# Performance work log

Hardware: AMD Instinct MI355X
Metric: run time of the kernel (lower is better)

## Reference

```python
import jax, jax.numpy as jnp
import numpy as np

H = 8          # num_heads
CHUNK = 68     # tokens_per_chunk = blocks_per_chunk(4) * tokens_per_block(17)
EPS = 1e-5


def _layer_norm(t, w, b):
    m = t.mean(-1, keepdims=True)
    v = t.var(-1, keepdims=True)
    return (t - m) / jnp.sqrt(v + EPS) * w + b


def _forward(tokens, embedding, Wq, bq, Wk, bk, Wv, bv, Wg, bg, Wo, bo,
             gn_w, gn_b, ln1_w, ln1_b, ln2_w, ln2_b, w1, b1, w2, b2):
    B, S = tokens.shape
    L, D, _ = Wq.shape
    dh = D // H
    n_chunks = S // CHUNK

    x = embedding[tokens]  # [B,S,D]

    # per-head decay gammas (standard RetNet)
    gamma = 1.0 - 2.0 ** (-5.0 - jnp.arange(H, dtype=jnp.float32))  # [H]

    # rotary relative-position tables (absolute positions, fresh state n=0)
    pos = jnp.arange(S, dtype=jnp.float32)
    inv = 1.0 / (10000.0 ** (jnp.arange(0, dh, 2, dtype=jnp.float32) / dh))
    ang = pos[:, None] * inv[None, :]                      # [S, dh/2]
    cs = jnp.concatenate([jnp.cos(ang)] * 2, -1)[None, :, None, :]  # [1,S,1,dh]
    sn = jnp.concatenate([jnp.sin(ang)] * 2, -1)[None, :, None, :]

    def rot(t):  # t: [B,S,H,dh]
        t1, t2 = jnp.split(t, 2, axis=-1)
        return t * cs + jnp.concatenate([-t2, t1], -1) * sn

    # chunkwise decay structures
    idx = jnp.arange(CHUNK, dtype=jnp.float32)
    expo = idx[:, None] - idx[None, :]
    Dmask = jnp.where(expo >= 0, gamma[:, None, None] ** expo[None], 0.0)  # [H,C,C]
    cross_dec = gamma[None, :] ** (idx[:, None] + 1.0)          # [C,H]
    k_dec = gamma[None, :] ** (CHUNK - 1.0 - idx[:, None])      # [C,H]
    chunk_dec = gamma ** CHUNK                                  # [H]

    for l in range(L):
        h = _layer_norm(x, ln1_w[l], ln1_b[l])
        q = rot((h @ Wq[l] + bq[l]).reshape(B, S, H, dh))
        k = rot((h @ Wk[l] + bk[l]).reshape(B, S, H, dh)) * (dh ** -0.5)
        v = (h @ Wv[l] + bv[l]).reshape(B, S, H, dh)
        # split into chunks, scan carries the per-head KV state [B,H,dh,dh]
        qc = q.reshape(B, n_chunks, CHUNK, H, dh).transpose(1, 0, 2, 3, 4)
        kc = k.reshape(B, n_chunks, CHUNK, H, dh).transpose(1, 0, 2, 3, 4)
        vc = v.reshape(B, n_chunks, CHUNK, H, dh).transpose(1, 0, 2, 3, 4)

        def step(state, qkv):
            qq, kk, vv = qkv  # each [B,C,H,dh]
            inner = jnp.einsum('bihd,bjhd->bhij', qq, kk) * Dmask
            out = jnp.einsum('bhij,bjhd->bihd', inner, vv)
            out = out + jnp.einsum('bihd,bhde->bihe', qq, state) * cross_dec[None, :, :, None]
            state = state * chunk_dec[None, :, None, None] + \
                jnp.einsum('bjhd,bjhe->bhde', kk * k_dec[None, :, :, None], vv)
            return state, out

        state0 = jnp.zeros((B, H, dh, dh), dtype=x.dtype)
        _, ret = jax.lax.scan(step, state0, (qc, kc, vc))
        ret = ret.transpose(1, 0, 2, 3, 4).reshape(B, S, H, dh)
        # per-head group norm
        m = ret.mean(-1, keepdims=True)
        vr = ret.var(-1, keepdims=True)
        ret = (ret - m) / jnp.sqrt(vr + EPS)
        ret = (ret * gn_w[l].reshape(H, dh) + gn_b[l].reshape(H, dh)).reshape(B, S, D)
        g = jax.nn.silu(h @ Wg[l] + bg[l])
        x = x + (g * ret) @ Wo[l] + bo[l]
        h2 = _layer_norm(x, ln2_w[l], ln2_b[l])
        x = x + jax.nn.silu(h2 @ w1[l] + b1[l]) @ w2[l] + b2[l]
    return x


def setup_inputs() -> dict:
    key = jax.random.key(0)
    B, S, D, L, FF, V = 16, 408, 512, 10, 2048, 519
    ks = jax.random.split(key, 16)
    r = lambda i, shape, s=0.02: jax.random.normal(ks[i], shape, dtype=jnp.float32) * s
    return {
        'tokens': jax.random.randint(ks[0], (B, S), 0, V, dtype=jnp.int32),
        'embedding': r(1, (V, D)),
        'Wq': r(2, (L, D, D)), 'bq': jnp.zeros((L, D), jnp.float32),
        'Wk': r(3, (L, D, D)), 'bk': jnp.zeros((L, D), jnp.float32),
        'Wv': r(4, (L, D, D)), 'bv': jnp.zeros((L, D), jnp.float32),
        'Wg': r(5, (L, D, D)), 'bg': jnp.zeros((L, D), jnp.float32),
        'Wo': r(6, (L, D, D)), 'bo': jnp.zeros((L, D), jnp.float32),
        'gn_w': jnp.ones((L, D), jnp.float32), 'gn_b': jnp.zeros((L, D), jnp.float32),
        'ln1_w': jnp.ones((L, D), jnp.float32), 'ln1_b': jnp.zeros((L, D), jnp.float32),
        'ln2_w': jnp.ones((L, D), jnp.float32), 'ln2_b': jnp.zeros((L, D), jnp.float32),
        'w1': r(7, (L, D, FF)), 'b1': jnp.zeros((L, FF), jnp.float32),
        'w2': r(8, (L, FF, D)), 'b2': jnp.zeros((L, D), jnp.float32),
    }


def reference(tokens, embedding, Wq, bq, Wk, bk, Wv, bv, Wg, bg, Wo, bo,
              gn_w, gn_b, ln1_w, ln1_b, ln2_w, ln2_b, w1, b1, w2, b2):
    return _forward(tokens, embedding, Wq, bq, Wk, bk, Wv, bv, Wg, bg, Wo, bo,
                    gn_w, gn_b, ln1_w, ln1_b, ln2_w, ln2_b, w1, b1, w2, b2)
```

## Files before the change

kernel.cpp:

```cpp
#include <hip/hip_runtime.h>
#include <hip/hip_bf16.h>

#define H 8
#define DH 64
#define DMODEL 512
#define SEQ 408
#define BATCH 16
#define NLAYER 10
#define FFDIM 2048
#define CHUNK 68
#define NCHUNK 6
#define M (BATCH*SEQ)
#define EPS 1e-5f

typedef __hip_bfloat16 bf16;
typedef unsigned short ushort_t;
typedef short bf8v __attribute__((ext_vector_type(8)));
typedef float f4v  __attribute__((ext_vector_type(4)));

__device__ __forceinline__ float us2f(unsigned short u){ return __uint_as_float(((unsigned)u) << 16); }
__device__ __forceinline__ unsigned short f2bfs(float f){
  __bf16 h = (__bf16)f;
  return *(unsigned short*)&h;
}
__device__ __forceinline__ void split2(float f, unsigned short& hi, unsigned short& lo){
  hi = f2bfs(f);
  lo = f2bfs(f - us2f(hi));
}

__global__ void embed_kernel(const int* __restrict__ tokens, const float* __restrict__ emb,
                             float* __restrict__ x){
  int idx = blockIdx.x*256 + threadIdx.x;
  if (idx >= M*DMODEL) return;
  int r = idx >> 9; int d = idx & 511;
  x[idx] = emb[(size_t)tokens[r]*DMODEL + d];
}

__global__ __launch_bounds__(256) void ln_kernel(const float* __restrict__ x,
    const float* __restrict__ w, const float* __restrict__ b,
    ushort_t* __restrict__ hhi, ushort_t* __restrict__ hlo){
  __shared__ float red[8];
  int r = blockIdx.x, tid = threadIdx.x;
  size_t base = (size_t)r*DMODEL;
  float v0 = x[base + tid], v1 = x[base + tid + 256];
  float s = v0 + v1, s2 = v0*v0 + v1*v1;
  int lane = tid & 63, wv = tid >> 6;
  #pragma unroll
  for (int o = 32; o; o >>= 1){ s += __shfl_xor(s, o); s2 += __shfl_xor(s2, o); }
  if (lane == 0){ red[wv] = s; red[wv+4] = s2; }
  __syncthreads();
  float tot  = red[0]+red[1]+red[2]+red[3];
  float tot2 = red[4]+red[5]+red[6]+red[7];
  float mean = tot * (1.0f/512.0f);
  float var  = tot2 * (1.0f/512.0f) - mean*mean;
  float rinv = rsqrtf(var + EPS);
  float o0 = (v0-mean)*rinv*w[tid]     + b[tid];
  float o1 = (v1-mean)*rinv*w[tid+256] + b[tid+256];
  unsigned short hi, lo;
  split2(o0, hi, lo); hhi[base+tid] = hi; hlo[base+tid] = lo;
  split2(o1, hi, lo); hhi[base+tid+256] = hi; hlo[base+tid+256] = lo;
}

#define BN 128
#define BK 32
#define LDK 40

template<int TBM>
__global__ __launch_bounds__(256) void gemm_mfma_kernel(
    const ushort_t* __restrict__ Ahi, const ushort_t* __restrict__ Alo,
    const float* __restrict__ W, const float* __restrict__ bias,
    const float* Cin, float* Cout, ushort_t* Co_hi, ushort_t* Co_lo,
    int N, int K, int epi)
{
  constexpr int TM = TBM/32;
  __shared__ __align__(16) short AsH[TBM*LDK];
  __shared__ __align__(16) short AsL[TBM*LDK];
  __shared__ __align__(16) short BsH[BN*LDK];
  __shared__ __align__(16) short BsL[BN*LDK];
  int tid = threadIdx.x;
  int lane = tid & 63, wave = tid >> 6;
  int wm = (wave >> 1) * (TBM/2), wn = (wave & 1) * 64;
  int l15 = lane & 15, quad = lane >> 4;
  int bm = blockIdx.y * TBM, bn = blockIdx.x * BN;

  f4v acc[TM][4];
  #pragma unroll
  for (int i = 0; i < TM; i++)
    #pragma unroll
    for (int j = 0; j < 4; j++) acc[i][j] = (f4v){0.f,0.f,0.f,0.f};

  int arow, akseg;
  if (TBM == 128){ arow = tid >> 1; akseg = (tid & 1) * 16; }
  else           { arow = tid >> 2; akseg = (tid & 3) * 8;  }
  int bnn = tid & 127, bkseg = (tid >> 7) * 16;

  for (int k0 = 0; k0 < K; k0 += BK){
    if (TBM == 128){
      const uint4* ap = (const uint4*)(Ahi + (size_t)(bm + arow)*K + k0 + akseg);
      uint4 a0 = ap[0], a1 = ap[1];
      *(uint4*)&AsH[arow*LDK + akseg]     = a0;
      *(uint4*)&AsH[arow*LDK + akseg + 8] = a1;
      const uint4* lp = (const uint4*)(Alo + (size_t)(bm + arow)*K + k0 + akseg);
      uint4 l0 = lp[0], l1 = lp[1];
      *(uint4*)&AsL[arow*LDK + akseg]     = l0;
      *(uint4*)&AsL[arow*LDK + akseg + 8] = l1;
    } else {
      uint4 a0 = *(const uint4*)(Ahi + (size_t)(bm + arow)*K + k0 + akseg);
      *(uint4*)&AsH[arow*LDK + akseg] = a0;
      uint4 l0 = *(const uint4*)(Alo + (size_t)(bm + arow)*K + k0 + akseg);
      *(uint4*)&AsL[arow*LDK + akseg] = l0;
    }
    size_t wbase = (size_t)(k0 + bkseg)*N + bn + bnn;
    unsigned short whi[16], wlo[16];
    #pragma unroll
    for (int i = 0; i < 16; i++) split2(W[wbase + (size_t)i*N], whi[i], wlo[i]);
    unsigned* bh = (unsigned*)&BsH[bnn*LDK + bkseg];
    unsigned* bl = (unsigned*)&BsL[bnn*LDK + bkseg];
    #pragma unroll
    for (int i = 0; i < 8; i++){
      bh[i] = (unsigned)whi[2*i] | ((unsigned)whi[2*i+1] << 16);
      bl[i] = (unsigned)wlo[2*i] | ((unsigned)wlo[2*i+1] << 16);
    }
    __syncthreads();
    bf8v afh[TM], afl[TM], bfh[4], bfl[4];
    #pragma unroll
    for (int t = 0; t < TM; t++){
      afh[t] = *(const bf8v*)&AsH[(wm + t*16 + l15)*LDK + quad*8];
      afl[t] = *(const bf8v*)&AsL[(wm + t*16 + l15)*LDK + quad*8];
    }
    #pragma unroll
    for (int t = 0; t < 4; t++){
      bfh[t] = *(const bf8v*)&BsH[(wn + t*16 + l15)*LDK + quad*8];
      bfl[t] = *(const bf8v*)&BsL[(wn + t*16 + l15)*LDK + quad*8];
    }
    #pragma unroll
    for (int i = 0; i < TM; i++)
      #pragma unroll
      for (int j = 0; j < 4; j++){
        acc[i][j] = __builtin_amdgcn_mfma_f32_16x16x32_bf16(afh[i], bfl[j], acc[i][j], 0, 0, 0);
        acc[i][j] = __builtin_amdgcn_mfma_f32_16x16x32_bf16(afl[i], bfh[j], acc[i][j], 0, 0, 0);
        acc[i][j] = __builtin_amdgcn_mfma_f32_16x16x32_bf16(afh[i], bfh[j], acc[i][j], 0, 0, 0);
      }
    __syncthreads();
  }
  #pragma unroll
  for (int i = 0; i < TM; i++){
    int m0 = bm + wm + i*16 + quad*4;
    #pragma unroll
    for (int j = 0; j < 4; j++){
      int n = bn + wn + j*16 + l15;
      float bsv = bias[n];
      #pragma unroll
      for (int r = 0; r < 4; r++){
        int m = m0 + r;
        float c = acc[i][j][r] + bsv;
        if (epi == 1) c = c / (1.0f + expf(-c));
        if (epi == 2) c += Cin[(size_t)m*N + n];
        if (Co_hi){
          unsigned short hi, lo; split2(c, hi, lo);
          Co_hi[(size_t)m*N + n] = hi;
          Co_lo[(size_t)m*N + n] = lo;
        } else {
          Cout[(size_t)m*N + n] = c;
        }
      }
    }
  }
}

__global__ __launch_bounds__(256) void gemm_qkvg_kernel(
    const ushort_t* __restrict__ Ahi, const ushort_t* __restrict__ Alo,
    const float* __restrict__ Wq, const float* __restrict__ Wk,
    const float* __restrict__ Wv, const float* __restrict__ Wg,
    const float* __restrict__ bq, const float* __restrict__ bk,
    const float* __restrict__ bv, const float* __restrict__ bg,
    float* __restrict__ qo, float* __restrict__ ko,
    float* __restrict__ vo, float* __restrict__ go)
{
  const int N = DMODEL, K = DMODEL;
  __shared__ __align__(16) short AsH[128*LDK];
  __shared__ __align__(16) short AsL[128*LDK];
  __shared__ __align__(16) short BsH[BN*LDK];
  __shared__ __align__(16) short BsL[BN*LDK];
  int tid = threadIdx.x;
  int lane = tid & 63, wave = tid >> 6;
  int wm = (wave >> 1) * 64, wn = (wave & 1) * 64;
  int l15 = lane & 15, quad = lane >> 4;
  int which = blockIdx.x >> 2;
  int bn = (blockIdx.x & 3) * BN;
  int bm = blockIdx.y * 128;
  const float* W    = (which==0) ? Wq : (which==1) ? Wk : (which==2) ? Wv : Wg;
  const float* bias = (which==0) ? bq : (which==1) ? bk : (which==2) ? bv : bg;
  float* out        = (which==0) ? qo : (which==1) ? ko : (which==2) ? vo : go;

  f4v acc[4][4];
  #pragma unroll
  for (int i = 0; i < 4; i++)
    #pragma unroll
    for (int j = 0; j < 4; j++) acc[i][j] = (f4v){0.f,0.f,0.f,0.f};

  int arow = tid >> 1, akseg = (tid & 1) * 16;
  int bnn = tid & 127, bkseg = (tid >> 7) * 16;

  for (int k0 = 0; k0 < K; k0 += BK){
    {
      const uint4* ap = (const uint4*)(Ahi + (size_t)(bm + arow)*K + k0 + akseg);
      uint4 a0 = ap[0], a1 = ap[1];
      *(uint4*)&AsH[arow*LDK + akseg]     = a0;
      *(uint4*)&AsH[arow*LDK + akseg + 8] = a1;
      const uint4* lp = (const uint4*)(Alo + (size_t)(bm + arow)*K + k0 + akseg);
      uint4 l0 = lp[0], l1 = lp[1];
      *(uint4*)&AsL[arow*LDK + akseg]     = l0;
      *(uint4*)&AsL[arow*LDK + akseg + 8] = l1;
    }
    size_t wbase = (size_t)(k0 + bkseg)*N + bn + bnn;
    unsigned short whi[16], wlo[16];
    #pragma unroll
    for (int i = 0; i < 16; i++) split2(W[wbase + (size_t)i*N], whi[i], wlo[i]);
    unsigned* bh = (unsigned*)&BsH[bnn*LDK + bkseg];
    unsigned* bl = (unsigned*)&BsL[bnn*LDK + bkseg];
    #pragma unroll
    for (int i = 0; i < 8; i++){
      bh[i] = (unsigned)whi[2*i] | ((unsigned)whi[2*i+1] << 16);
      bl[i] = (unsigned)wlo[2*i] | ((unsigned)wlo[2*i+1] << 16);
    }
    __syncthreads();
    bf8v afh[4], afl[4], bfh[4], bfl[4];
    #pragma unroll
    for (int t = 0; t < 4; t++){
      afh[t] = *(const bf8v*)&AsH[(wm + t*16 + l15)*LDK + quad*8];
      afl[t] = *(const bf8v*)&AsL[(wm + t*16 + l15)*LDK + quad*8];
      bfh[t] = *(const bf8v*)&BsH[(wn + t*16 + l15)*LDK + quad*8];
      bfl[t] = *(const bf8v*)&BsL[(wn + t*16 + l15)*LDK + quad*8];
    }
    #pragma unroll
    for (int i = 0; i < 4; i++)
      #pragma unroll
      for (int j = 0; j < 4; j++){
        acc[i][j] = __builtin_amdgcn_mfma_f32_16x16x32_bf16(afh[i], bfl[j], acc[i][j], 0, 0, 0);
        acc[i][j] = __builtin_amdgcn_mfma_f32_16x16x32_bf16(afl[i], bfh[j], acc[i][j], 0, 0, 0);
        acc[i][j] = __builtin_amdgcn_mfma_f32_16x16x32_bf16(afh[i], bfh[j], acc[i][j], 0, 0, 0);
      }
    __syncthreads();
  }
  #pragma unroll
  for (int i = 0; i < 4; i++){
    int m0 = bm + wm + i*16 + quad*4;
    #pragma unroll
    for (int j = 0; j < 4; j++){
      int n = bn + wn + j*16 + l15;
      float bsv = bias[n];
      #pragma unroll
      for (int r = 0; r < 4; r++){
        int m = m0 + r;
        float c = acc[i][j][r] + bsv;
        if (which == 3) c = c / (1.0f + expf(-c));
        out[(size_t)m*N + n] = c;
      }
    }
  }
}

__global__ void rope_kernel(float* __restrict__ q, float* __restrict__ k){
  int idx = blockIdx.x*256 + threadIdx.x;
  if (idx >= M*256) return;
  int r = idx >> 8, p = idx & 255;
  int hh = p >> 5, i = p & 31;
  int s = r % SEQ;
  float inv = powf(10000.0f, -(float)(2*i) * (1.0f/64.0f));
  float ang = (float)s * inv;
  float sn, c; sincosf(ang, &sn, &c);
  size_t base = (size_t)r*DMODEL + hh*64 + i;
  float q1 = q[base], q2 = q[base+32];
  q[base]    = q1*c - q2*sn;
  q[base+32] = q2*c + q1*sn;
  float k1 = k[base], k2 = k[base+32];
  const float sc = 0.125f;
  k[base]    = (k1*c - k2*sn)*sc;
  k[base+32] = (k2*c + k1*sn)*sc;
}

__global__ __launch_bounds__(256) void ret_chunkkv_kernel(
    const float* __restrict__ k, const float* __restrict__ v, float* __restrict__ Ast)
{
  __shared__ __align__(16) float kT[DH][CHUNK];
  __shared__ __align__(16) float vs[CHUNK][DH];
  __shared__ float gpw[CHUNK];
  int tid = threadIdx.x;
  int c = blockIdx.x % NCHUNK;
  int bh = blockIdx.x / NCHUNK;
  int hh = bh & 7, b = bh >> 3;
  float gamma = 1.0f - exp2f(-5.0f - (float)hh);
  if (tid < CHUNK) gpw[tid] = powf(gamma, (float)(CHUNK-1-tid));
  size_t rowbase = ((size_t)(b*SEQ + c*CHUNK))*DMODEL + hh*DH;
  for (int e = tid; e < CHUNK*DH; e += 256){
    int i = e >> 6, d = e & 63;
    size_t g = rowbase + (size_t)i*DMODEL + d;
    kT[d][i] = k[g];
    vs[i][d] = v[g];
  }
  __syncthreads();
  float* A = Ast + (size_t)blockIdx.x * (DH*DH);
  for (int e = tid; e < DH*16; e += 256){
    int d = e >> 4, q4 = (e & 15) * 4;
    float4 a4 = {0,0,0,0};
    for (int j = 0; j < CHUNK; j++){
      float kj = kT[d][j] * gpw[j];
      float4 v4 = *(const float4*)&vs[j][q4];
      a4.x += kj*v4.x; a4.y += kj*v4.y; a4.z += kj*v4.z; a4.w += kj*v4.w;
    }
    *(float4*)&A[d*DH + q4] = a4;
  }
}

__global__ __launch_bounds__(256) void ret_scan_kernel(float* __restrict__ Ast)
{
  int bh = blockIdx.x, hh = bh & 7;
  float gamma = 1.0f - exp2f(-5.0f - (float)hh);
  float chdec = powf(gamma, (float)CHUNK);
  int tid = threadIdx.x;
  float4 run[4];
  #pragma unroll
  for (int t = 0; t < 4; t++) run[t] = (float4){0,0,0,0};
  size_t base = (size_t)bh * NCHUNK * (DH*DH) + (size_t)tid*16;
  for (int c = 0; c < NCHUNK; c++){
    float4* slot = (float4*)(Ast + base + (size_t)c*(DH*DH));
    float4 a[4];
    #pragma unroll
    for (int t = 0; t < 4; t++) a[t] = slot[t];
    #pragma unroll
    for (int t = 0; t < 4; t++) slot[t] = run[t];
    #pragma unroll
    for (int t = 0; t < 4; t++){
      run[t].x = run[t].x*chdec + a[t].x;
      run[t].y = run[t].y*chdec + a[t].y;
      run[t].z = run[t].z*chdec + a[t].z;
      run[t].w = run[t].w*chdec + a[t].w;
    }
  }
}

__global__ __launch_bounds__(256) void ret_out_kernel(
    const float* __restrict__ q, const float* __restrict__ k, const float* __restrict__ v,
    const float* __restrict__ Ast, float* __restrict__ ret)
{
  __shared__ __align__(16) float qs[CHUNK][DH];
  __shared__ __align__(16) float kT[DH][CHUNK];
  __shared__ __align__(16) float vs[CHUNK][DH];
  __shared__ __align__(16) float sts[DH*DH];
  __shared__ float inner[34][CHUNK];
  __shared__ float gpw[CHUNK];
  int tid = threadIdx.x;
  int c = blockIdx.x % NCHUNK;
  int bh = blockIdx.x / NCHUNK;
  int hh = bh & 7, b = bh >> 3;
  float gamma = 1.0f - exp2f(-5.0f - (float)hh);
  if (tid < CHUNK) gpw[tid] = powf(gamma, (float)tid);
  size_t rowbase = ((size_t)(b*SEQ + c*CHUNK))*DMODEL + hh*DH;
  for (int e = tid; e < CHUNK*DH; e += 256){
    int i = e >> 6, d = e & 63;
    size_t g = rowbase + (size_t)i*DMODEL + d;
    qs[i][d] = q[g];
    kT[d][i] = k[g];
    vs[i][d] = v[g];
  }
  const float* st = Ast + (size_t)blockIdx.x * (DH*DH);
  for (int e = tid*4; e < DH*DH; e += 1024)
    *(float4*)&sts[e] = *(const float4*)&st[e];
  __syncthreads();
  for (int p = 0; p < 2; p++){
    int i0 = p*34;
    for (int e = tid; e < 34*CHUNK; e += 256){
      int ii = e / CHUNK, j = e - ii*CHUNK;
      int i = i0 + ii;
      float val = 0.0f;
      if (j <= i){
        float dot = 0.0f;
        #pragma unroll 16
        for (int d = 0; d < DH; d++) dot += qs[i][d] * kT[d][j];
        val = dot * gpw[i-j];
      }
      inner[ii][j] = val;
    }
    __syncthreads();
    for (int e = tid; e < 34*16; e += 256){
      int ii = e >> 4, q4 = (e & 15) * 4;
      int i = i0 + ii;
      float4 o4 = {0,0,0,0};
      for (int j = 0; j <= i; j++){
        float w = inner[ii][j];
        float4 v4 = *(const float4*)&vs[j][q4];
        o4.x += w*v4.x; o4.y += w*v4.y; o4.z += w*v4.z; o4.w += w*v4.w;
      }
      float4 c4 = {0,0,0,0};
      #pragma unroll 8
      for (int e2 = 0; e2 < DH; e2++){
        float qv = qs[i][e2];
        float4 s4 = *(const float4*)&sts[e2*DH + q4];
        c4.x += qv*s4.x; c4.y += qv*s4.y; c4.z += qv*s4.z; c4.w += qv*s4.w;
      }
      float cd = gpw[i] * gamma;
      size_t ob = rowbase + (size_t)i*DMODEL + q4;
      float4 o; o.x = o4.x + cd*c4.x; o.y = o4.y + cd*c4.y;
      o.z = o4.z + cd*c4.z; o.w = o4.w + cd*c4.w;
      *(float4*)&ret[ob] = o;
    }
    __syncthreads();
  }
}

__global__ __launch_bounds__(512) void gnorm_gate_kernel(const float* __restrict__ ret,
    const float* __restrict__ g, const float* __restrict__ gnw, const float* __restrict__ gnb,
    ushort_t* __restrict__ ohi, ushort_t* __restrict__ olo)
{
  int r = blockIdx.x, tid = threadIdx.x;
  size_t idx = (size_t)r*DMODEL + tid;
  float val = ret[idx];
  float s = val, s2 = val*val;
  #pragma unroll
  for (int o = 32; o; o >>= 1){ s += __shfl_xor(s, o); s2 += __shfl_xor(s2, o); }
  float mean = s * (1.0f/64.0f);
  float var  = s2 * (1.0f/64.0f) - mean*mean;
  float y = (val - mean) * rsqrtf(var + EPS);
  y = y * gnw[tid] + gnb[tid];
  y = y * g[idx];
  unsigned short hi, lo; split2(y, hi, lo);
  ohi[idx] = hi; olo[idx] = lo;
}

__global__ void outwrite_kernel(const float* __restrict__ x, float* __restrict__ out){
  int idx = blockIdx.x*256 + threadIdx.x;
  if (idx < M*DMODEL) out[idx] = x[idx];
}

extern "C" void kernel_launch(void* const* d_in, const int* in_sizes, int n_in,
                              void* d_out, int out_size, void* d_ws, size_t ws_size,
                              hipStream_t stream)
{
  (void)in_sizes; (void)n_in; (void)out_size; (void)ws_size;
  const int*   tokens = (const int*)d_in[0];
  const float* emb  = (const float*)d_in[1];
  const float* Wq = (const float*)d_in[2];  const float* bq = (const float*)d_in[3];
  const float* Wk = (const float*)d_in[4];  const float* bk = (const float*)d_in[5];
  const float* Wv = (const float*)d_in[6];  const float* bv = (const float*)d_in[7];
  const float* Wg = (const float*)d_in[8];  const float* bg = (const float*)d_in[9];
  const float* Wo = (const float*)d_in[10]; const float* bo = (const float*)d_in[11];
  const float* gnw = (const float*)d_in[12]; const float* gnb = (const float*)d_in[13];
  const float* ln1w = (const float*)d_in[14]; const float* ln1b = (const float*)d_in[15];
  const float* ln2w = (const float*)d_in[16]; const float* ln2b = (const float*)d_in[17];
  const float* w1 = (const float*)d_in[18]; const float* b1 = (const float*)d_in[19];
  const float* w2 = (const float*)d_in[20]; const float* b2 = (const float*)d_in[21];

  const size_t MD = (size_t)M*DMODEL;
  float* xf = (float*)d_ws;
  float* qf = xf + MD;
  float* kf = qf + MD;
  float* vf = kf + MD;
  float* gf = vf + MD;
  float* rf = gf + MD;
  ushort_t* h_hi = (ushort_t*)(rf + MD);
  ushort_t* h_lo = h_hi + MD;
  float* Ast = (float*)h_hi;
  ushort_t* rg_hi = h_hi;
  ushort_t* rg_lo = h_lo;
  ushort_t* ff_hi = (ushort_t*)qf;
  ushort_t* ff_lo = (ushort_t*)vf;

  embed_kernel<<<(M*DMODEL)/256, 256, 0, stream>>>(tokens, emb, xf);

  dim3 gqkvg(16, M/128);
  dim3 g512b(DMODEL/BN, M/64);
  dim3 gff(FFDIM/BN, M/128);
  for (int l = 0; l < NLAYER; l++){
    const size_t wO = (size_t)l*DMODEL*DMODEL;
    const size_t bO = (size_t)l*DMODEL;
    const size_t w1O = (size_t)l*DMODEL*FFDIM;
    const size_t b1O = (size_t)l*FFDIM;
    ln_kernel<<<M, 256, 0, stream>>>(xf, ln1w + bO, ln1b + bO, h_hi, h_lo);
    gemm_qkvg_kernel<<<gqkvg, 256, 0, stream>>>(h_hi, h_lo,
        Wq + wO, Wk + wO, Wv + wO, Wg + wO,
        bq + bO, bk + bO, bv + bO, bg + bO,
        qf, kf, vf, gf);
    rope_kernel<<<M, 256, 0, stream>>>(qf, kf);
    ret_chunkkv_kernel<<<BATCH*H*NCHUNK, 256, 0, stream>>>(kf, vf, Ast);
    ret_scan_kernel<<<BATCH*H, 256, 0, stream>>>(Ast);
    ret_out_kernel<<<BATCH*H*NCHUNK, 256, 0, stream>>>(qf, kf, vf, Ast, rf);
    gnorm_gate_kernel<<<M, 512, 0, stream>>>(rf, gf, gnw + bO, gnb + bO, rg_hi, rg_lo);
    gemm_mfma_kernel<64><<<g512b, 256, 0, stream>>>(rg_hi, rg_lo, Wo + wO, bo + bO, xf, xf, nullptr, nullptr, DMODEL, DMODEL, 2);
    ln_kernel<<<M, 256, 0, stream>>>(xf, ln2w + bO, ln2b + bO, h_hi, h_lo);
    gemm_mfma_kernel<128><<<gff, 256, 0, stream>>>(h_hi, h_lo, w1 + w1O, b1 + b1O, nullptr, nullptr, ff_hi, ff_lo, FFDIM, DMODEL, 1);
    gemm_mfma_kernel<64><<<g512b, 256, 0, stream>>>(ff_hi, ff_lo, w2 + w1O, b2 + bO, xf, xf, nullptr, nullptr, DMODEL, FFDIM, 2);
  }
  outwrite_kernel<<<(M*DMODEL)/256, 256, 0, stream>>>(xf, (float*)d_out);
}
```

Measured before the change: 4.202 ms.

## Pre-split weights into transposed bf16 hi/lo buffers and prefetch GEMM tiles

Adds per-layer kernels that convert each fp32 weight matrix once into transposed bf16 hi/lo arrays in a workspace. Every GEMM block previously repeated this conversion with strided, uncoalesced loads. The GEMMs now load pre-split weights with vectorized 16-byte reads and register-prefetch the next K tile while computing the current one. The cost is extra split kernel launches and workspace traffic each layer, and the workspace aliases the rf buffer, so its lifetime must not overlap the retention output.

After: 4.126 ms. No clear change (-1.8%).

```diff
diff --git a/kernel.cpp b/kernel.cpp
--- a/kernel.cpp
+++ b/kernel.cpp
@@ -17,6 +17,15 @@
 typedef unsigned short ushort_t;
 typedef short bf8v __attribute__((ext_vector_type(8)));
 typedef float f4v  __attribute__((ext_vector_type(4)));
+
+static constexpr size_t QKVG_STRIDE = 2u*512*512;
+static constexpr size_t QKVG_HL     = 512*512;
+static constexpr size_t WO_HI = 0;
+static constexpr size_t WO_LO = WO_HI + 512*512;
+static constexpr size_t W1_HI = WO_LO + 512*512;
+static constexpr size_t W1_LO = W1_HI + 2048*512;
+static constexpr size_t W2_HI = W1_LO + 2048*512;
+static constexpr size_t W2_LO = W2_HI + 512*2048;
 
 __device__ __forceinline__ float us2f(unsigned short u){ return __uint_as_float(((unsigned)u) << 16); }
 __device__ __forceinline__ unsigned short f2bfs(float f){
@@ -61,14 +70,66 @@
   split2(o1, hi, lo); hhi[base+tid+256] = hi; hlo[base+tid+256] = lo;
 }
 
+__device__ __forceinline__ void wsplit_tile(const float* __restrict__ W,
+    ushort_t* __restrict__ hi, ushort_t* __restrict__ lo,
+    int N, int K, int n0, int k0)
+{
+  __shared__ float tb[32][33];
+  int tx = threadIdx.x & 31, ty = threadIdx.x >> 5;
+  #pragma unroll
+  for (int r = 0; r < 32; r += 8)
+    tb[ty+r][tx] = W[(size_t)(k0+ty+r)*N + n0 + tx];
+  __syncthreads();
+  #pragma unroll
+  for (int r = 0; r < 32; r += 8){
+    float v = tb[tx][ty+r];
+    unsigned short h, l; split2(v, h, l);
+    size_t o = (size_t)(n0+ty+r)*K + k0 + tx;
+    hi[o] = h; lo[o] = l;
+  }
+}
+
+__global__ __launch_bounds__(256) void wsplit_qkvg_kernel(
+    const float* __restrict__ Wq, const float* __restrict__ Wk,
+    const float* __restrict__ Wv, const float* __restrict__ Wg,
+    ushort_t* __restrict__ wsp)
+{
+  int z = blockIdx.z;
+  const float* W = (z==0)?Wq:(z==1)?Wk:(z==2)?Wv:Wg;
+  ushort_t* hi = wsp + (size_t)z*QKVG_STRIDE;
+  wsplit_tile(W, hi, hi + QKVG_HL, 512, 512, blockIdx.x*32, blockIdx.y*32);
+}
+
+__global__ __launch_bounds__(256) void wsplit_ffo_kernel(
+    const float* __restrict__ Wo, const float* __restrict__ w1,
+    const float* __restrict__ w2, ushort_t* __restrict__ wsp)
+{
+  int b = blockIdx.x;
+  const float* W; ushort_t* hi; int N, K, n0, k0;
+  if (b < 256){
+    W = Wo; hi = wsp + WO_HI; N = 512; K = 512;
+    n0 = (b & 15)*32; k0 = (b >> 4)*32;
+  } else if (b < 1280){
+    int bb = b - 256;
+    W = w1; hi = wsp + W1_HI; N = 2048; K = 512;
+    n0 = (bb & 63)*32; k0 = (bb >> 6)*32;
+  } else {
+    int bb = b - 1280;
+    W = w2; hi = wsp + W2_HI; N = 512; K = 2048;
+    n0 = (bb & 15)*32; k0 = (bb >> 4)*32;
+  }
+  wsplit_tile(W, hi, hi + (size_t)N*K, N, K, n0, k0);
+}
+
 #define BN 128
 #define BK 32
 #define LDK 40
 
 template<int TBM>
-__global__ __launch_bounds__(256) void gemm_mfma_kernel(
+__global__ __launch_bounds__(256) void gemm_ps_kernel(
     const ushort_t* __restrict__ Ahi, const ushort_t* __restrict__ Alo,
-    const float* __restrict__ W, const float* __restrict__ bias,
+    const ushort_t* __restrict__ Bhi, const ushort_t* __restrict__ Blo,
+    const float* __restrict__ bias,
     const float* Cin, float* Cout, ushort_t* Co_hi, ushort_t* Co_lo,
     int N, int K, int epi)
 {
@@ -94,44 +155,45 @@
   else           { arow = tid >> 2; akseg = (tid & 3) * 8;  }
   int bnn = tid & 127, bkseg = (tid >> 7) * 16;
 
-  for (int k0 = 0; k0 < K; k0 += BK){
+  const ushort_t* aH = Ahi + (size_t)(bm + arow)*K + akseg;
+  const ushort_t* aL = Alo + (size_t)(bm + arow)*K + akseg;
+  const ushort_t* bH = Bhi + (size_t)(bn + bnn)*K + bkseg;
+  const ushort_t* bL = Blo + (size_t)(bn + bnn)*K + bkseg;
+
+  uint4 rAh0, rAh1, rAl0, rAl1, rBh0, rBh1, rBl0, rBl1;
+#define GLOAD_PS(k0) do{ \
+    rAh0 = *(const uint4*)(aH + (k0)); \
+    rAl0 = *(const uint4*)(aL + (k0)); \
+    if (TBM == 128){ rAh1 = *(const uint4*)(aH + (k0) + 8); \
+                     rAl1 = *(const uint4*)(aL + (k0) + 8); } \
+    rBh0 = *(const uint4*)(bH + (k0));     rBh1 = *(const uint4*)(bH + (k0) + 8); \
+    rBl0 = *(const uint4*)(bL + (k0));     rBl1 = *(const uint4*)(bL + (k0) + 8); \
+  }while(0)
+
+  GLOAD_PS(0);
+  const int nt = K / BK;
+  for (int t = 0; t < nt; t++){
+    __syncthreads();
+    *(uint4*)&AsH[arow*LDK + akseg] = rAh0;
+    *(uint4*)&AsL[arow*LDK + akseg] = rAl0;
     if (TBM == 128){
-      const uint4* ap = (const uint4*)(Ahi + (size_t)(bm + arow)*K + k0 + akseg);
-      uint4 a0 = ap[0], a1 = ap[1];
-      *(uint4*)&AsH[arow*LDK + akseg]     = a0;
-      *(uint4*)&AsH[arow*LDK + akseg + 8] = a1;
-      const uint4* lp = (const uint4*)(Alo + (size_t)(bm + arow)*K + k0 + akseg);
-      uint4 l0 = lp[0], l1 = lp[1];
-      *(uint4*)&AsL[arow*LDK + akseg]     = l0;
-      *(uint4*)&AsL[arow*LDK + akseg + 8] = l1;
-    } else {
-      uint4 a0 = *(const uint4*)(Ahi + (size_t)(bm + arow)*K + k0 + akseg);
-      *(uint4*)&AsH[arow*LDK + akseg] = a0;
-      uint4 l0 = *(const uint4*)(Alo + (size_t)(bm + arow)*K + k0 + akseg);
-      *(uint4*)&AsL[arow*LDK + akseg] = l0;
-    }
-    size_t wbase = (size_t)(k0 + bkseg)*N + bn + bnn;
-    unsigned short whi[16], wlo[16];
-    #pragma unroll
-    for (int i = 0; i < 16; i++) split2(W[wbase + (size_t)i*N], whi[i], wlo[i]);
-    unsigned* bh = (unsigned*)&BsH[bnn*LDK + bkseg];
-    unsigned* bl = (unsigned*)&BsL[bnn*LDK + bkseg];
-    #pragma unroll
-    for (int i = 0; i < 8; i++){
-      bh[i] = (unsigned)whi[2*i] | ((unsigned)whi[2*i+1] << 16);
-      bl[i] = (unsigned)wlo[2*i] | ((unsigned)wlo[2*i+1] << 16);
-    }
+      *(uint4*)&AsH[arow*LDK + akseg + 8] = rAh1;
+      *(uint4*)&AsL[arow*LDK + akseg + 8] = rAl1;
+    }
+    *(uint4*)&BsH[bnn*LDK + bkseg] = rBh0; *(uint4*)&BsH[bnn*LDK + bkseg + 8] = rBh1;
+    *(uint4*)&BsL[bnn*LDK + bkseg] = rBl0; *(uint4*)&BsL[bnn*LDK + bkseg + 8] = rBl1;
     __syncthreads();
+    if (t + 1 < nt) GLOAD_PS((t+1)*BK);
     bf8v afh[TM], afl[TM], bfh[4], bfl[4];
     #pragma unroll
-    for (int t = 0; t < TM; t++){
-      afh[t] = *(const bf8v*)&AsH[(wm + t*16 + l15)*LDK + quad*8];
-      afl[t] = *(const bf8v*)&AsL[(wm + t*16 + l15)*LDK + quad*8];
-    }
-    #pragma unroll
-    for (int t = 0; t < 4; t++){
-      bfh[t] = *(const bf8v*)&BsH[(wn + t*16 + l15)*LDK + quad*8];
-      bfl[t] = *(const bf8v*)&BsL[(wn + t*16 + l15)*LDK + quad*8];
+    for (int i = 0; i < TM; i++){
+      afh[i] = *(const bf8v*)&AsH[(wm + i*16 + l15)*LDK + quad*8];
+      afl[i] = *(const bf8v*)&AsL[(wm + i*16 + l15)*LDK + quad*8];
+    }
+    #pragma unroll
+    for (int j = 0; j < 4; j++){
+      bfh[j] = *(const bf8v*)&BsH[(wn + j*16 + l15)*LDK + quad*8];
+      bfl[j] = *(const bf8v*)&BsL[(wn + j*16 + l15)*LDK + quad*8];
     }
     #pragma unroll
     for (int i = 0; i < TM; i++)
@@ -141,8 +203,8 @@
         acc[i][j] = __builtin_amdgcn_mfma_f32_16x16x32_bf16(afl[i], bfh[j], acc[i][j], 0, 0, 0);
         acc[i][j] = __builtin_amdgcn_mfma_f32_16x16x32_bf16(afh[i], bfh[j], acc[i][j], 0, 0, 0);
       }
-    __syncthreads();
-  }
+  }
+#undef GLOAD_PS
   #pragma unroll
   for (int i = 0; i < TM; i++){
     int m0 = bm + wm + i*16 + quad*4;
@@ -170,8 +232,7 @@
 
 __global__ __launch_bounds__(256) void gemm_qkvg_kernel(
     const ushort_t* __restrict__ Ahi, const ushort_t* __restrict__ Alo,
-    const float* __restrict__ Wq, const float* __restrict__ Wk,
-    const float* __restrict__ Wv, const float* __restrict__ Wg,
+    const ushort_t* __restrict__ wsp,
     const float* __restrict__ bq, const float* __restrict__ bk,
     const float* __restrict__ bv, const float* __restrict__ bg,
     float* __restrict__ qo, float* __restrict__ ko,
@@ -189,7 +250,8 @@
   int which = blockIdx.x >> 2;
   int bn = (blockIdx.x & 3) * BN;
   int bm = blockIdx.y * 128;
-  const float* W    = (which==0) ? Wq : (which==1) ? Wk : (which==2) ? Wv : Wg;
+  const ushort_t* Bhi = wsp + (size_t)which * QKVG_STRIDE;
+  const ushort_t* Blo = Bhi + QKVG_HL;
   const float* bias = (which==0) ? bq : (which==1) ? bk : (which==2) ? bv : bg;
   float* out        = (which==0) ? qo : (which==1) ? ko : (which==2) ? vo : go;
 
@@ -202,36 +264,38 @@
   int arow = tid >> 1, akseg = (tid & 1) * 16;
   int bnn = tid & 127, bkseg = (tid >> 7) * 16;
 
-  for (int k0 = 0; k0 < K; k0 += BK){
-    {
-      const uint4* ap = (const uint4*)(Ahi + (size_t)(bm + arow)*K + k0 + akseg);
-      uint4 a0 = ap[0], a1 = ap[1];
-      *(uint4*)&AsH[arow*LDK + akseg]     = a0;
-      *(uint4*)&AsH[arow*LDK + akseg + 8] = a1;
-      const uint4* lp = (const uint4*)(Alo + (size_t)(bm + arow)*K + k0 + akseg);
-      uint4 l0 = lp[0], l1 = lp[1];
-      *(uint4*)&AsL[arow*LDK + akseg]     = l0;
-      *(uint4*)&AsL[arow*LDK + akseg + 8] = l1;
-    }
-    size_t wbase = (size_t)(k0 + bkseg)*N + bn + bnn;
-    unsigned short whi[16], wlo[16];
-    #pragma unroll
-    for (int i = 0; i < 16; i++) split2(W[wbase + (size_t)i*N], whi[i], wlo[i]);
-    unsigned* bh = (unsigned*)&BsH[bnn*LDK + bkseg];
-    unsigned* bl = (unsigned*)&BsL[bnn*LDK + bkseg];
-    #pragma unroll
-    for (int i = 0; i < 8; i++){
-      bh[i] = (unsigned)whi[2*i] | ((unsigned)whi[2*i+1] << 16);
-      bl[i] = (unsigned)wlo[2*i] | ((unsigned)wlo[2*i+1] << 16);
-    }
+  const ushort_t* aH = Ahi + (size_t)(bm + arow)*K + akseg;
+  const ushort_t* aL = Alo + (size_t)(bm + arow)*K + akseg;
+  const ushort_t* bH = Bhi + (size_t)(bn + bnn)*K + bkseg;
+  const ushort_t* bL = Blo + (size_t)(bn + bnn)*K + bkseg;
+
+  uint4 rAh0, rAh1, rAl0, rAl1, rBh0, rBh1, rBl0, rBl1;
+#define GLOADQ(k0) do{ \
+    rAh0 = *(const uint4*)(aH + (k0)); rAh1 = *(const uint4*)(aH + (k0) + 8); \
+    rAl0 = *(const uint4*)(aL + (k0)); rAl1 = *(const uint4*)(aL + (k0) + 8); \
+    rBh0 = *(const uint4*)(bH + (k0)); rBh1 = *(const uint4*)(bH + (k0) + 8); \
+    rBl0 = *(const uint4*)(bL + (k0)); rBl1 = *(const uint4*)(bL + (k0) + 8); \
+  }while(0)
+
+  GLOADQ(0);
+  const int nt = K / BK;
+  for (int t = 0; t < nt; t++){
     __syncthreads();
+    *(uint4*)&AsH[arow*LDK + akseg]     = rAh0;
+    *(uint4*)&AsH[arow*LDK + akseg + 8] = rAh1;
+    *(uint4*)&AsL[arow*LDK + akseg]     = rAl0;
+    *(uint4*)&AsL[arow*LDK + akseg + 8] = rAl1;
+    *(uint4*)&BsH[bnn*LDK + bkseg] = rBh0; *(uint4*)&BsH[bnn*LDK + bkseg + 8] = rBh1;
+    *(uint4*)&BsL[bnn*LDK + bkseg] = rBl0; *(uint4*)&BsL[bnn*LDK + bkseg + 8] = rBl1;
+    __syncthreads();
+    if (t + 1 < nt) GLOADQ((t+1)*BK);
     bf8v afh[4], afl[4], bfh[4], bfl[4];
     #pragma unroll
-    for (int t = 0; t < 4; t++){
-      afh[t] = *(const bf8v*)&AsH[(wm + t*16 + l15)*LDK + quad*8];
-      afl[t] = *(const bf8v*)&AsL[(wm + t*16 + l15)*LDK + quad*8];
-      bfh[t] = *(const bf8v*)&BsH[(wn + t*16 + l15)*LDK + quad*8];
-      bfl[t] = *(const bf8v*)&BsL[(wn + t*16 + l15)*LDK + quad*8];
+    for (int i = 0; i < 4; i++){
+      afh[i] = *(const bf8v*)&AsH[(wm + i*16 + l15)*LDK + quad*8];
+      afl[i] = *(const bf8v*)&AsL[(wm + i*16 + l15)*LDK + quad*8];
+      bfh[i] = *(const bf8v*)&BsH[(wn + i*16 + l15)*LDK + quad*8];
+      bfl[i] = *(const bf8v*)&BsL[(wn + i*16 + l15)*LDK + quad*8];
     }
     #pragma unroll
     for (int i = 0; i < 4; i++)
@@ -241,8 +305,8 @@
         acc[i][j] = __builtin_amdgcn_mfma_f32_16x16x32_bf16(afl[i], bfh[j], acc[i][j], 0, 0, 0);
         acc[i][j] = __builtin_amdgcn_mfma_f32_16x16x32_bf16(afh[i], bfh[j], acc[i][j], 0, 0, 0);
       }
-    __syncthreads();
-  }
+  }
+#undef GLOADQ
   #pragma unroll
   for (int i = 0; i < 4; i++){
     int m0 = bm + wm + i*16 + quad*4;
@@ -465,20 +529,22 @@
   ushort_t* rg_lo = h_lo;
   ushort_t* ff_hi = (ushort_t*)qf;
   ushort_t* ff_lo = (ushort_t*)vf;
+  ushort_t* wsp = (ushort_t*)rf;
 
   embed_kernel<<<(M*DMODEL)/256, 256, 0, stream>>>(tokens, emb, xf);
 
   dim3 gqkvg(16, M/128);
   dim3 g512b(DMODEL/BN, M/64);
   dim3 gff(FFDIM/BN, M/128);
+  dim3 gsplit4(16, 16, 4);
   for (int l = 0; l < NLAYER; l++){
     const size_t wO = (size_t)l*DMODEL*DMODEL;
     const size_t bO = (size_t)l*DMODEL;
     const size_t w1O = (size_t)l*DMODEL*FFDIM;
     const size_t b1O = (size_t)l*FFDIM;
+    wsplit_qkvg_kernel<<<gsplit4, 256, 0, stream>>>(Wq + wO, Wk + wO, Wv + wO, Wg + wO, wsp);
     ln_kernel<<<M, 256, 0, stream>>>(xf, ln1w + bO, ln1b + bO, h_hi, h_lo);
-    gemm_qkvg_kernel<<<gqkvg, 256, 0, stream>>>(h_hi, h_lo,
-        Wq + wO, Wk + wO, Wv + wO, Wg + wO,
+    gemm_qkvg_kernel<<<gqkvg, 256, 0, stream>>>(h_hi, h_lo, wsp,
         bq + bO, bk + bO, bv + bO, bg + bO,
         qf, kf, vf, gf);
     rope_kernel<<<M, 256, 0, stream>>>(qf, kf);
@@ -486,10 +552,14 @@
     ret_scan_kernel<<<BATCH*H, 256, 0, stream>>>(Ast);
     ret_out_kernel<<<BATCH*H*NCHUNK, 256, 0, stream>>>(qf, kf, vf, Ast, rf);
     gnorm_gate_kernel<<<M, 512, 0, stream>>>(rf, gf, gnw + bO, gnb + bO, rg_hi, rg_lo);
-    gemm_mfma_kernel<64><<<g512b, 256, 0, stream>>>(rg_hi, rg_lo, Wo + wO, bo + bO, xf, xf, nullptr, nullptr, DMODEL, DMODEL, 2);
+    wsplit_ffo_kernel<<<2304, 256, 0, stream>>>(Wo + wO, w1 + w1O, w2 + w1O, wsp);
+    gemm_ps_kernel<64><<<g512b, 256, 0, stream>>>(rg_hi, rg_lo,
+        wsp + WO_HI, wsp + WO_LO, bo + bO, xf, xf, nullptr, nullptr, DMODEL, DMODEL, 2);
     ln_kernel<<<M, 256, 0, stream>>>(xf, ln2w + bO, ln2b + bO, h_hi, h_lo);
-    gemm_mfma_kernel<128><<<gff, 256, 0, stream>>>(h_hi, h_lo, w1 + w1O, b1 + b1O, nullptr, nullptr, ff_hi, ff_lo, FFDIM, DMODEL, 1);
-    gemm_mfma_kernel<64><<<g512b, 256, 0, stream>>>(ff_hi, ff_lo, w2 + w1O, b2 + bO, xf, xf, nullptr, nullptr, DMODEL, FFDIM, 2);
+    gemm_ps_kernel<128><<<gff, 256, 0, stream>>>(h_hi, h_lo,
+        wsp + W1_HI, wsp + W1_LO, b1 + b1O, nullptr, nullptr, ff_hi, ff_lo, FFDIM, DMODEL, 1);
+    gemm_ps_kernel<64><<<g512b, 256, 0, stream>>>(ff_hi, ff_lo,
+        wsp + W2_HI, wsp + W2_LO, b2 + bO, xf, xf, nullptr, nullptr, DMODEL, FFDIM, 2);
   }
   outwrite_kernel<<<(M*DMODEL)/256, 256, 0, stream>>>(xf, (float*)d_out);
 }
```
